# Kernel tuning notes

Measured on AMD Instinct MI355X. Metric: run time of the kernel, lower is better.

The kernel has to match this reference:

```python
import jax, jax.numpy as jnp
import numpy as np

B, S, E, H, FF = 4, 1024, 1024, 16, 4096
D = E // H
EPS = 1e-5


def layer_norm(x, g, b):
    m = jnp.mean(x, axis=-1, keepdims=True)
    v = jnp.var(x, axis=-1, keepdims=True)
    return (x - m) / jnp.sqrt(v + EPS) * g + b


def setup_inputs() -> dict:
    key = jax.random.key(0)
    ks = jax.random.split(key, 12)
    x = jax.random.normal(ks[0], (B, S, E), dtype=jnp.float32)
    # binary attention mask [B,S,S]; force diagonal=1 so no row is fully masked
    mask = jax.random.randint(ks[1], (B, S, S), 0, 2).astype(jnp.float32)
    idx = jnp.arange(S)
    mask = mask.at[:, idx, idx].set(1.0)
    gnn_adj = jax.random.normal(ks[2], (B, S, S), dtype=jnp.float32) * 0.02
    sc = 0.02
    params = dict(
        Wq=jax.random.normal(ks[3], (E, E), dtype=jnp.float32) * sc, bq=jnp.zeros((E,), jnp.float32),
        Wk=jax.random.normal(ks[4], (E, E), dtype=jnp.float32) * sc, bk=jnp.zeros((E,), jnp.float32),
        Wv=jax.random.normal(ks[5], (E, E), dtype=jnp.float32) * sc, bv=jnp.zeros((E,), jnp.float32),
        Wo=jax.random.normal(ks[6], (E, E), dtype=jnp.float32) * sc, bo=jnp.zeros((E,), jnp.float32),
        g1=jnp.ones((E,), jnp.float32), b1=jnp.zeros((E,), jnp.float32),
        g2=jnp.ones((E,), jnp.float32), b2=jnp.zeros((E,), jnp.float32),
        W1=jax.random.normal(ks[7], (E, FF), dtype=jnp.float32) * sc, bf1=jnp.zeros((FF,), jnp.float32),
        W2=jax.random.normal(ks[8], (FF, E), dtype=jnp.float32) * sc, bf2=jnp.zeros((E,), jnp.float32),
    )
    return dict(x=x, mask=mask, gnn_adj=gnn_adj, **params)


def reference(x, mask, gnn_adj, Wq, bq, Wk, bk, Wv, bv, Wo, bo, g1, b1, g2, b2, W1, bf1, W2, bf2):
    # pre-norm (norm_first=True), dropout = identity (eval)
    nx = layer_norm(x, g1, b1)
    # QKV projections -> [B,H,S,D]
    def split_heads(t):
        return t.reshape(B, S, H, D).transpose(0, 2, 1, 3)
    q = split_heads(nx @ Wq + bq)
    k = split_heads(nx @ Wk + bk)
    v = split_heads(nx @ Wv + bv)
    scores = jnp.einsum('bhqd,bhkd->bhqk', q, k) / jnp.sqrt(jnp.float32(D))
    m = mask[:, None]  # [B,1,S,S]
    scores = jnp.where(m == 0, -jnp.inf, scores * m)
    attn = jax.nn.softmax(scores, axis=-1)
    # non-standard: additive bias AFTER softmax
    attn = attn + gnn_adj[:, None]
    xv = jnp.einsum('bhqk,bhkd->bhqd', attn, v)
    xv = xv.transpose(0, 2, 1, 3).reshape(B, S, E)
    x = x + (xv @ Wo + bo)
    h = layer_norm(x, g2, b2)
    ff = jax.nn.gelu(h @ W1 + bf1, approximate=False) @ W2 + bf2
    return x + ff
```

## Files before the change

### kernel.cpp

```cpp
#include <hip/hip_runtime.h>
#include <hip/hip_bf16.h>

typedef unsigned short u16;
typedef short bf16x8 __attribute__((ext_vector_type(8)));
typedef float f32x4 __attribute__((ext_vector_type(4)));

#define B_ 4
#define S_ 1024
#define E_ 1024
#define H_ 16
#define FF_ 4096
#define D_ 64
#define M_ 4096

__device__ __forceinline__ u16 f2bf(float f) {
  unsigned int u = __builtin_bit_cast(unsigned int, f);
  u += 0x7fffu + ((u >> 16) & 1u);
  return (u16)(u >> 16);
}
__device__ __forceinline__ float bf2f(u16 v) {
  unsigned int u = ((unsigned int)v) << 16;
  return __builtin_bit_cast(float, u);
}

__device__ __forceinline__ void gld_lds16(const void* g, void* l) {
  __builtin_amdgcn_global_load_lds((__attribute__((address_space(1))) void*)g,
                                   (__attribute__((address_space(3))) void*)l,
                                   16, 0, 0);
}

__global__ void __launch_bounds__(256) pre_kernel(
    const float* __restrict__ wq, const float* __restrict__ wk,
    const float* __restrict__ wv, const float* __restrict__ wo,
    const float* __restrict__ w1, const float* __restrict__ w2,
    u16* __restrict__ wt,
    const float* __restrict__ x, const float* __restrict__ g1,
    const float* __restrict__ b1, u16* __restrict__ nx,
    const float* __restrict__ mask, const float* __restrict__ gnn,
    u16* __restrict__ biasI, u16* __restrict__ gnnbf) {
  __shared__ __attribute__((aligned(16))) float smem_f[1088];
  int bid = blockIdx.x;
  int t = threadIdx.x;
  if (bid < 12288) {
    const float* src; u16* dst; int K, N; int local;
    if (bid < 4096) {
      int wsel = bid >> 10; local = bid & 1023; K = 1024; N = 1024;
      src = wsel == 0 ? wq : wsel == 1 ? wk : wsel == 2 ? wv : wo;
      dst = wt + (size_t)wsel * 1024 * 1024;
    } else if (bid < 8192) {
      local = bid - 4096; K = 1024; N = 4096; src = w1;
      dst = wt + (size_t)4 * 1024 * 1024;
    } else {
      local = bid - 8192; K = 4096; N = 1024; src = w2;
      dst = wt + (size_t)8 * 1024 * 1024;
    }
    int tiles_n = N >> 5;
    int n0 = (local % tiles_n) << 5, k0 = (local / tiles_n) << 5;
    float (*tl)[33] = reinterpret_cast<float(*)[33]>(smem_f);
    int tx = t & 31, ty = t >> 5;
#pragma unroll
    for (int i = 0; i < 4; ++i)
      tl[ty + i * 8][tx] = src[(size_t)(k0 + ty + i * 8) * N + n0 + tx];
    __syncthreads();
#pragma unroll
    for (int i = 0; i < 4; ++i)
      dst[(size_t)(n0 + ty + i * 8) * K + k0 + tx] = f2bf(tl[tx][ty + i * 8]);
  } else if (bid < 16384) {
    int row = bid - 12288;
    const float* xr = x + (size_t)row * 1024;
    float4 v = *(const float4*)(xr + t * 4);
    float s = v.x + v.y + v.z + v.w;
    float q = v.x * v.x + v.y * v.y + v.z * v.z + v.w * v.w;
#pragma unroll
    for (int off = 1; off < 64; off <<= 1) {
      s += __shfl_xor(s, off);
      q += __shfl_xor(q, off);
    }
    float* sb = smem_f;
    float* qb = smem_f + 4;
    int w = t >> 6, l = t & 63;
    if (l == 0) { sb[w] = s; qb[w] = q; }
    __syncthreads();
    s = sb[0] + sb[1] + sb[2] + sb[3];
    q = qb[0] + qb[1] + qb[2] + qb[3];
    float mean = s * (1.f / 1024.f);
    float var = q * (1.f / 1024.f) - mean * mean;
    float rs = rsqrtf(var + 1e-5f);
    float4 gv = *(const float4*)(g1 + t * 4);
    float4 bv = *(const float4*)(b1 + t * 4);
    ushort4 o;
    o.x = f2bf((v.x - mean) * rs * gv.x + bv.x);
    o.y = f2bf((v.y - mean) * rs * gv.y + bv.y);
    o.z = f2bf((v.z - mean) * rs * gv.z + bv.z);
    o.w = f2bf((v.w - mean) * rs * gv.w + bv.w);
    *(ushort4*)(nx + (size_t)row * 1024 + t * 4) = o;
  } else {
    int row = bid - 16384;
    int b = row >> 10, q = row & 1023;
    float* mrow = smem_f;
    const float* mp = mask + ((size_t)row << 10);
    const float* gp = gnn + ((size_t)row << 10);
    float4 mv = *(const float4*)(mp + t * 4);
    *(float4*)(mrow + t * 4) = mv;
    float4 gv = *(const float4*)(gp + t * 4);
    ushort4 g4;
    g4.x = f2bf(gv.x); g4.y = f2bf(gv.y); g4.z = f2bf(gv.z); g4.w = f2bf(gv.w);
    *(ushort4*)(gnnbf + ((size_t)row << 10) + t * 4) = g4;
    __syncthreads();
    int kt = t >> 4, c = t & 15;
    const u16 NEG = f2bf(-30008.f);
    const u16 SHIFT = f2bf(-8.0f);
    ushort4 o;
    o.x = (mrow[kt * 64 + c] == 0.f) ? NEG : SHIFT;
    o.y = (mrow[kt * 64 + 16 + c] == 0.f) ? NEG : SHIFT;
    o.z = (mrow[kt * 64 + 32 + c] == 0.f) ? NEG : SHIFT;
    o.w = (mrow[kt * 64 + 48 + c] == 0.f) ? NEG : SHIFT;
    *(ushort4*)(biasI + (((size_t)(b * 16 + kt) << 10) + q) * 64 + c * 4) = o;
  }
}

__global__ void __launch_bounds__(256) vtrans_kernel(
    const u16* __restrict__ v, u16* __restrict__ vt) {
  int st = blockIdx.x, h = blockIdx.y, b = blockIdx.z;
  __shared__ u16 tl[64][72];
  const u16* src = v + ((((size_t)(b * 16 + h)) << 10) + (st << 6)) * 64;
  int r = threadIdx.x >> 2, g = (threadIdx.x & 3) << 4;
  *(uint4*)&tl[r][g] = *(const uint4*)(src + r * 64 + g);
  *(uint4*)&tl[r][g + 8] = *(const uint4*)(src + r * 64 + g + 8);
  __syncthreads();
  u16 tmp[16];
#pragma unroll
  for (int i = 0; i < 16; ++i) tmp[i] = tl[g + i][r];
  u16* dst = vt + ((size_t)b << 20) + (((size_t)(h * 64 + r)) << 10) + (st << 6) + g;
  *(uint4*)(dst) = *(uint4*)(tmp);
  *(uint4*)(dst + 8) = *(uint4*)(tmp + 8);
}

__global__ void __launch_bounds__(256) ln_kernel_b(
    const u16* __restrict__ x, const float* __restrict__ g,
    const float* __restrict__ bt, u16* __restrict__ out) {
  int row = blockIdx.x, t = threadIdx.x;
  const u16* xr = x + ((size_t)row << 10);
  ushort4 xv4 = *(const ushort4*)(xr + t * 4);
  float v0 = bf2f(xv4.x), v1 = bf2f(xv4.y), v2 = bf2f(xv4.z), v3 = bf2f(xv4.w);
  float s = v0 + v1 + v2 + v3;
  float q = v0 * v0 + v1 * v1 + v2 * v2 + v3 * v3;
#pragma unroll
  for (int off = 1; off < 64; off <<= 1) {
    s += __shfl_xor(s, off);
    q += __shfl_xor(q, off);
  }
  __shared__ float sb[4], qb[4];
  int w = t >> 6, l = t & 63;
  if (l == 0) { sb[w] = s; qb[w] = q; }
  __syncthreads();
  s = sb[0] + sb[1] + sb[2] + sb[3];
  q = qb[0] + qb[1] + qb[2] + qb[3];
  float mean = s * (1.f / 1024.f);
  float var = q * (1.f / 1024.f) - mean * mean;
  float rs = rsqrtf(var + 1e-5f);
  float4 gv = *(const float4*)(g + t * 4);
  float4 bv = *(const float4*)(bt + t * 4);
  ushort4 o;
  o.x = f2bf((v0 - mean) * rs * gv.x + bv.x);
  o.y = f2bf((v1 - mean) * rs * gv.y + bv.y);
  o.z = f2bf((v2 - mean) * rs * gv.z + bv.z);
  o.w = f2bf((v3 - mean) * rs * gv.w + bv.w);
  *(ushort4*)(out + ((size_t)row << 10) + t * 4) = o;
}

template <int LDA, int LDB, int NKT>
__device__ __forceinline__ void gemm_core_db64(
    const u16* __restrict__ A, const u16* __restrict__ Bt,
    int bm, int bn, u16* lds, f32x4 acc[4][2]) {
  const int tid = threadIdx.x;
  const int w = tid >> 6, l = tid & 63;
  const int wn = w << 5;
  const int lrow = l >> 3;
  const int cg = (l & 7) ^ lrow;
  const u16* Ab = A + (size_t)(bm << 6) * LDA + (cg << 3);
  const u16* Bb = Bt + (size_t)(bn << 7) * LDB + (cg << 3);
#define GSTAGE64(T, BUF)                                                     \
  {                                                                          \
    const int kk = (T) << 6;                                                 \
    u16* la = lds + (BUF) * 12288;                                           \
    u16* lb = la + 4096;                                                     \
    _Pragma("unroll") for (int i = 0; i < 2; ++i) {                          \
      int c = (w << 1) + i;                                                  \
      int row = (c << 3) + lrow;                                             \
      gld_lds16(Ab + (size_t)row * LDA + kk, la + (c << 9));                 \
    }                                                                        \
    _Pragma("unroll") for (int i = 0; i < 4; ++i) {                          \
      int c = (w << 2) + i;                                                  \
      int row = (c << 3) + lrow;                                             \
      gld_lds16(Bb + (size_t)row * LDB + kk, lb + (c << 9));                 \
    }                                                                        \
  }
  GSTAGE64(0, 0);
  __syncthreads();
  for (int t = 0; t < NKT; ++t) {
    if (t + 1 < NKT) GSTAGE64(t + 1, (t & 1) ^ 1);
    const u16* la = lds + (t & 1) * 12288;
    const u16* lb = la + 4096;
    bf16x8 af[2][4], bfr[2][2];
    const int rr = l & 15;
    const int kgb = l >> 4;
#pragma unroll
    for (int ks = 0; ks < 2; ++ks) {
      const int kg = kgb + (ks << 2);
#pragma unroll
      for (int f = 0; f < 4; ++f) {
        int ra = (f << 4) + rr;
        af[ks][f] = *(const bf16x8*)(la + (ra << 6) + ((kg ^ (ra & 7)) << 3));
      }
#pragma unroll
      for (int f = 0; f < 2; ++f) {
        int rb = wn + (f << 4) + rr;
        bfr[ks][f] = *(const bf16x8*)(lb + (rb << 6) + ((kg ^ (rb & 7)) << 3));
      }
    }
#pragma unroll
    for (int fm = 0; fm < 4; ++fm)
#pragma unroll
      for (int fn = 0; fn < 2; ++fn)
#pragma unroll
        for (int ks = 0; ks < 2; ++ks)
          acc[fm][fn] = __builtin_amdgcn_mfma_f32_16x16x32_bf16(
              af[ks][fm], bfr[ks][fn], acc[fm][fn], 0, 0, 0);
    __syncthreads();
  }
#undef GSTAGE64
}

template <int LDA, int LDB, int NKT>
__device__ __forceinline__ void gemm_core_p3(
    const u16* __restrict__ A, const u16* __restrict__ Bt,
    int bm, int bn, u16* lds, f32x4 acc[4][2]) {
  const int tid = threadIdx.x;
  const int w = tid >> 6, l = tid & 63;
  const int wn = w << 5;
  const int lrow = l >> 3;
  const int cg = (l & 7) ^ lrow;
  const u16* Ab = A + (size_t)(bm << 6) * LDA + (cg << 3);
  const u16* Bb = Bt + (size_t)(bn << 7) * LDB + (cg << 3);
#define PSTAGE(T, BUF)                                                       \
  {                                                                          \
    const int kk = (T) << 6;                                                 \
    u16* la = lds + (BUF) * 12288;                                           \
    u16* lb = la + 4096;                                                     \
    _Pragma("unroll") for (int i = 0; i < 2; ++i) {                          \
      int c = (w << 1) + i;                                                  \
      int row = (c << 3) + lrow;                                             \
      gld_lds16(Ab + (size_t)row * LDA + kk, la + (c << 9));                 \
    }                                                                        \
    _Pragma("unroll") for (int i = 0; i < 4; ++i) {                          \
      int c = (w << 2) + i;                                                  \
      int row = (c << 3) + lrow;                                             \
      gld_lds16(Bb + (size_t)row * LDB + kk, lb + (c << 9));                 \
    }                                                                        \
  }
  PSTAGE(0, 0);
  PSTAGE(1, 1);
  int cur = 0;
  for (int t = 0; t < NKT; ++t) {
    if (t + 2 < NKT) {
      int nb = cur + 2; if (nb >= 3) nb -= 3;
      PSTAGE(t + 2, nb);
      asm volatile("s_waitcnt vmcnt(12)" ::: "memory");
    } else if (t + 1 < NKT) {
      asm volatile("s_waitcnt vmcnt(6)" ::: "memory");
    } else {
      asm volatile("s_waitcnt vmcnt(0)" ::: "memory");
    }
    __builtin_amdgcn_sched_barrier(0);
    __builtin_amdgcn_s_barrier();
    const u16* la = lds + cur * 12288;
    const u16* lb = la + 4096;
    bf16x8 af[2][4], bfr[2][2];
    const int rr = l & 15;
    const int kgb = l >> 4;
#pragma unroll
    for (int ks = 0; ks < 2; ++ks) {
      const int kg = kgb + (ks << 2);
#pragma unroll
      for (int f = 0; f < 4; ++f) {
        int ra = (f << 4) + rr;
        af[ks][f] = *(const bf16x8*)(la + (ra << 6) + ((kg ^ (ra & 7)) << 3));
      }
#pragma unroll
      for (int f = 0; f < 2; ++f) {
        int rb = wn + (f << 4) + rr;
        bfr[ks][f] = *(const bf16x8*)(lb + (rb << 6) + ((kg ^ (rb & 7)) << 3));
      }
    }
    __builtin_amdgcn_s_setprio(1);
#pragma unroll
    for (int fm = 0; fm < 4; ++fm)
#pragma unroll
      for (int fn = 0; fn < 2; ++fn)
#pragma unroll
        for (int ks = 0; ks < 2; ++ks)
          acc[fm][fn] = __builtin_amdgcn_mfma_f32_16x16x32_bf16(
              af[ks][fm], bfr[ks][fn], acc[fm][fn], 0, 0, 0);
    __builtin_amdgcn_s_setprio(0);
    asm volatile("s_waitcnt lgkmcnt(0)" ::: "memory");
    __builtin_amdgcn_sched_barrier(0);
    __builtin_amdgcn_s_barrier();
    cur = (cur == 2) ? 0 : cur + 1;
  }
#undef PSTAGE
}

#define ACC_INIT64()                      \
  f32x4 acc[4][2];                        \
  { f32x4 zf = {0.f, 0.f, 0.f, 0.f};      \
_Pragma("unroll")                         \
    for (int a = 0; a < 4; ++a)           \
_Pragma("unroll")                         \
      for (int bb = 0; bb < 2; ++bb) acc[a][bb] = zf; }

#define EPI_SETUP64()                                   \
  const int w = threadIdx.x >> 6, l = threadIdx.x & 63; \
  const int wn = w << 5;

#define GEMM_LDS64()  __shared__ __attribute__((aligned(16))) u16 lds[2 * 12288]

__global__ void __launch_bounds__(256, 2) gemm_qkv(
    const u16* __restrict__ nx, const u16* __restrict__ wt,
    const float* __restrict__ bq, const float* __restrict__ bk,
    const float* __restrict__ bv, u16* __restrict__ qk, u16* __restrict__ vtmp) {
  GEMM_LDS64();
  ACC_INIT64();
  int z = blockIdx.z;
  const u16* Bt = wt + (size_t)z * 1024 * 1024;
  const float* bias = z == 0 ? bq : z == 1 ? bk : bv;
  u16* out = z == 2 ? vtmp : qk + (size_t)z * M_ * 1024;
  const float scl = (z == 0) ? 0.18033688f : 1.0f;
  gemm_core_db64<1024, 1024, 16>(nx, Bt, blockIdx.x, blockIdx.y, lds, acc);
  EPI_SETUP64();
#pragma unroll
  for (int fm = 0; fm < 4; ++fm)
#pragma unroll
    for (int fn = 0; fn < 2; ++fn)
#pragma unroll
      for (int j = 0; j < 4; ++j) {
        int row = (blockIdx.x << 6) + (fm << 4) + ((l >> 4) << 2) + j;
        int col = (blockIdx.y << 7) + wn + (fn << 4) + (l & 15);
        float v = (acc[fm][fn][j] + bias[col]) * scl;
        int b = row >> 10, s = row & 1023;
        int h = col >> 6, d = col & 63;
        out[(((size_t)(b * 16 + h) << 10) + s) * 64 + d] = f2bf(v);
      }
}

__global__ void __launch_bounds__(256, 2) gemm_gnnv(
    const u16* __restrict__ gnnbf, const u16* __restrict__ vt,
    u16* __restrict__ xvg) {
  GEMM_LDS64();
  ACC_INIT64();
  int b = blockIdx.z;
  const u16* A = gnnbf + ((size_t)b << 20);
  const u16* Bt = vt + ((size_t)b << 20);
  u16* out = xvg + ((size_t)b << 20);
  gemm_core_db64<1024, 1024, 16>(A, Bt, blockIdx.x, blockIdx.y, lds, acc);
  EPI_SETUP64();
#pragma unroll
  for (int fm = 0; fm < 4; ++fm)
#pragma unroll
    for (int fn = 0; fn < 2; ++fn)
#pragma unroll
      for (int j = 0; j < 4; ++j) {
        int row = (blockIdx.x << 6) + (fm << 4) + ((l >> 4) << 2) + j;
        int col = (blockIdx.y << 7) + wn + (fn << 4) + (l & 15);
        out[((size_t)row << 10) + col] = f2bf(acc[fm][fn][j]);
      }
}

__global__ void __launch_bounds__(256, 2) gemm_wo(
    const u16* __restrict__ xv, const u16* __restrict__ wt,
    const float* __restrict__ bo, const float* __restrict__ xres,
    u16* __restrict__ x1b) {
  GEMM_LDS64();
  ACC_INIT64();
  gemm_core_db64<1024, 1024, 16>(xv, wt, blockIdx.x, blockIdx.y, lds, acc);
  EPI_SETUP64();
#pragma unroll
  for (int fm = 0; fm < 4; ++fm)
#pragma unroll
    for (int fn = 0; fn < 2; ++fn)
#pragma unroll
      for (int j = 0; j < 4; ++j) {
        int row = (blockIdx.x << 6) + (fm << 4) + ((l >> 4) << 2) + j;
        int col = (blockIdx.y << 7) + wn + (fn << 4) + (l & 15);
        size_t idx = ((size_t)row << 10) + col;
        x1b[idx] = f2bf(acc[fm][fn][j] + bo[col] + xres[idx]);
      }
}

__global__ void __launch_bounds__(512, 1) gemm_w1_256p(
    const u16* __restrict__ hb, const u16* __restrict__ wt,
    const float* __restrict__ bf1, u16* __restrict__ ff1) {
  extern __shared__ __attribute__((aligned(16))) u16 lds[];
  const int bid = blockIdx.x;
  const int lin = ((bid & 7) << 5) + (bid >> 3);
  const int bm = lin & 15, bn = lin >> 4;
  const int tid = threadIdx.x;
  const int w = tid >> 6, l = tid & 63;
  const int wm = (w >> 2) << 7;
  const int wn = (w & 3) << 6;
  const int lrow3 = l >> 3;
  const int vsw = (l & 7) ^ lrow3;
  const int rpar = vsw >> 2, k8s = vsw & 3;
  const u16* Ab = hb + (size_t)(bm << 8) * 1024 + k8s * 8;
  const u16* Bb = wt + (size_t)(bn << 8) * 1024 + k8s * 8;

  f32x4 acc[8][4];
  {
    f32x4 zf = {0.f, 0.f, 0.f, 0.f};
#pragma unroll
    for (int a = 0; a < 8; ++a)
#pragma unroll
      for (int bb2 = 0; bb2 < 4; ++bb2) acc[a][bb2] = zf;
  }

#define WSTAGE(T, BUF)                                                       \
  {                                                                          \
    const int kk = (T) << 5;                                                 \
    u16* la = lds + (BUF) * 16384;                                           \
    u16* lb = la + 8192;                                                     \
    _Pragma("unroll") for (int i = 0; i < 2; ++i) {                          \
      int c = (w << 1) + i;                                                  \
      int row = ((c << 3) + lrow3) * 2 + rpar;                               \
      gld_lds16(Ab + (size_t)row * 1024 + kk, la + (c << 9) + (l << 3));     \
      gld_lds16(Bb + (size_t)row * 1024 + kk, lb + (c << 9) + (l << 3));     \
    }                                                                        \
  }

  WSTAGE(0, 0);
  WSTAGE(1, 1);
  int cur = 0;
  const int rr = l & 15;
  const int kg = l >> 4;
  for (int t = 0; t < 32; ++t) {
    if (t + 2 < 32) {
      int nb = cur + 2; if (nb >= 3) nb -= 3;
      WSTAGE(t + 2, nb);
      asm volatile("s_waitcnt vmcnt(8)" ::: "memory");
    } else if (t + 1 < 32) {
      asm volatile("s_waitcnt vmcnt(4)" ::: "memory");
    } else {
      asm volatile("s_waitcnt vmcnt(0)" ::: "memory");
    }
    __builtin_amdgcn_sched_barrier(0);
    __builtin_amdgcn_s_barrier();
    const u16* la = lds + cur * 16384;
    const u16* lb = la + 8192;
    bf16x8 bfr[4];
#pragma unroll
    for (int fn = 0; fn < 4; ++fn) {
      int rb = wn + (fn << 4) + rr;
      int slot = (((rb & 1) << 2) | kg) ^ ((rb >> 1) & 7);
      bfr[fn] = *(const bf16x8*)(lb + ((rb >> 1) << 6) + (slot << 3));
    }
    __builtin_amdgcn_s_setprio(1);
#pragma unroll
    for (int fm = 0; fm < 8; ++fm) {
      int ra = wm + (fm << 4) + rr;
      int slot = (((ra & 1) << 2) | kg) ^ ((ra >> 1) & 7);
      bf16x8 afr = *(const bf16x8*)(la + ((ra >> 1) << 6) + (slot << 3));
#pragma unroll
      for (int fn = 0; fn < 4; ++fn)
        acc[fm][fn] = __builtin_amdgcn_mfma_f32_16x16x32_bf16(
            afr, bfr[fn], acc[fm][fn], 0, 0, 0);
    }
    __builtin_amdgcn_s_setprio(0);
    asm volatile("s_waitcnt lgkmcnt(0)" ::: "memory");
    __builtin_amdgcn_sched_barrier(0);
    __builtin_amdgcn_s_barrier();
    cur = (cur == 2) ? 0 : cur + 1;
  }
#undef WSTAGE
#pragma unroll
  for (int fm = 0; fm < 8; ++fm)
#pragma unroll
    for (int fn = 0; fn < 4; ++fn)
#pragma unroll
      for (int j = 0; j < 4; ++j) {
        int row = (bm << 8) + wm + (fm << 4) + ((l >> 4) << 2) + j;
        int col = (bn << 8) + wn + (fn << 4) + (l & 15);
        float v = acc[fm][fn][j] + bf1[col];
        float ge = 0.5f * v * (1.f + erff(v * 0.70710678118654752f));
        ff1[((size_t)row << 12) + col] = f2bf(ge);
      }
}

__global__ void __launch_bounds__(256, 2) gemm_w2(
    const u16* __restrict__ ff1, const u16* __restrict__ wt,
    const float* __restrict__ bf2, const u16* __restrict__ x1b,
    float* __restrict__ out) {
  extern __shared__ __attribute__((aligned(16))) u16 lds[];
  ACC_INIT64();
  gemm_core_p3<4096, 4096, 64>(ff1, wt, blockIdx.x, blockIdx.y, lds, acc);
  EPI_SETUP64();
#pragma unroll
  for (int fm = 0; fm < 4; ++fm)
#pragma unroll
    for (int fn = 0; fn < 2; ++fn)
#pragma unroll
      for (int j = 0; j < 4; ++j) {
        int row = (blockIdx.x << 6) + (fm << 4) + ((l >> 4) << 2) + j;
        int col = (blockIdx.y << 7) + wn + (fn << 4) + (l & 15);
        size_t idx = ((size_t)row << 10) + col;
        out[idx] = acc[fm][fn][j] + bf2[col] + bf2f(x1b[idx]);
      }
}

__global__ void __launch_bounds__(256, 2) attn_kernel(
    const u16* __restrict__ Q, const u16* __restrict__ K,
    const u16* __restrict__ Vt, const u16* __restrict__ biasI,
    const u16* __restrict__ xvg, u16* __restrict__ xv) {
  const int lin = ((blockIdx.x & 7) << 6) + (blockIdx.x >> 3);
  const int qt = lin & 7, h = (lin >> 3) & 15, b = lin >> 7;
  const int tid = threadIdx.x, w = tid >> 6, l = tid & 63;
  __shared__ __attribute__((aligned(16))) u16 kbuf[2][64 * 64];
  __shared__ __attribute__((aligned(16))) u16 vbuf[2][64 * 64];
  __shared__ __attribute__((aligned(16))) u16 pbuf[4][32 * 64];
  const size_t bh = ((size_t)(b * 16 + h)) << 16;
  const u16* Qb = Q + bh;
  const u16* Kb = K + bh;
  const u16* Vtb = Vt + ((size_t)b << 20) + ((size_t)(h * 64) << 10);
  const u16* biasb = biasI + ((size_t)b << 20);
  const int q0 = (qt << 7) + (w << 5);
  const int lrow = l >> 3, cg = (l & 7) ^ lrow;
  const int l4 = l >> 4, lo = l & 15;
  u16* p_w = pbuf[w];

  bf16x8 qf[2][2];
#pragma unroll
  for (int m = 0; m < 2; ++m)
#pragma unroll
    for (int ks = 0; ks < 2; ++ks)
      qf[m][ks] = *(const bf16x8*)(Qb + ((size_t)(q0 + m * 16 + lo) << 6) +
                                   l4 * 8 + ks * 32);
  bf16x8 onesf;
#pragma unroll
  for (int j = 0; j < 8; ++j) onesf[j] = (short)0x3F80;

  f32x4 osoft[2][4], osum[2];
  f32x4 zf = {0.f, 0.f, 0.f, 0.f};
#pragma unroll
  for (int m = 0; m < 2; ++m) {
    osum[m] = zf;
#pragma unroll
    for (int fd = 0; fd < 4; ++fd) osoft[m][fd] = zf;
  }

#define STAGE(T, BUF)                                                          \
  {                                                                            \
    int kv0s = (T) << 6;                                                       \
    u16* kd = &kbuf[BUF][0];                                                   \
    u16* vd = &vbuf[BUF][0];                                                   \
    _Pragma("unroll") for (int i = 0; i < 2; ++i) {                            \
      int c = (w << 1) + i;                                                    \
      gld_lds16(Kb + ((size_t)(kv0s + (c << 3) + lrow) << 6) + (cg << 3),      \
                kd + (c << 9));                                                \
      gld_lds16(Vtb + ((size_t)((c << 3) + lrow) << 10) + kv0s + (cg << 3),    \
                vd + (c << 9));                                                \
    }                                                                          \
  }

  STAGE(0, 0);
  __syncthreads();

  for (int t = 0; t < 16; ++t) {
    const int cur = t & 1;
    if (t < 15) STAGE(t + 1, cur ^ 1);
    const u16* kb_ = &kbuf[cur][0];
    const u16* vb_ = &vbuf[cur][0];
    f32x4 sacc[2][4];
#pragma unroll
    for (int m = 0; m < 2; ++m)
#pragma unroll
      for (int j = 0; j < 4; ++j) {
        ushort4 bb = *(const ushort4*)(
            biasb + (((size_t)(t * 1024 + q0 + m * 16 + l4 * 4 + j)) << 6) +
            lo * 4);
        sacc[m][0][j] = bf2f(bb.x);
        sacc[m][1][j] = bf2f(bb.y);
        sacc[m][2][j] = bf2f(bb.z);
        sacc[m][3][j] = bf2f(bb.w);
      }
    __builtin_amdgcn_s_setprio(1);
#pragma unroll
    for (int ks = 0; ks < 2; ++ks) {
      const int kg = l4 + (ks << 2);
      bf16x8 kf[4];
#pragma unroll
      for (int fn = 0; fn < 4; ++fn) {
        int rk = (fn << 4) + lo;
        kf[fn] = *(const bf16x8*)(kb_ + (rk << 6) + ((kg ^ (rk & 7)) << 3));
      }
#pragma unroll
      for (int m = 0; m < 2; ++m)
#pragma unroll
        for (int fn = 0; fn < 4; ++fn)
          sacc[m][fn] = __builtin_amdgcn_mfma_f32_16x16x32_bf16(
              qf[m][ks], kf[fn], sacc[m][fn], 0, 0, 0);
    }
    __builtin_amdgcn_s_setprio(0);
#pragma unroll
    for (int m = 0; m < 2; ++m)
#pragma unroll
      for (int fn = 0; fn < 4; ++fn)
#pragma unroll
        for (int j = 0; j < 4; ++j) {
          float p = exp2f(sacc[m][fn][j]);
          unsigned int u = __builtin_bit_cast(unsigned int, p);
          int prow = (m << 4) + (l4 << 2) + j;
          int pcol = (fn << 4) + lo;
          p_w[(prow << 6) + (pcol ^ ((prow & 7) << 3))] =
              (u16)((u + 0x8000u) >> 16);
        }
    __builtin_amdgcn_s_setprio(1);
#pragma unroll
    for (int ks = 0; ks < 2; ++ks) {
      const int kg = l4 + (ks << 2);
      bf16x8 pf[2], vf[4];
#pragma unroll
      for (int m = 0; m < 2; ++m) {
        int pr = (m << 4) + lo;
        pf[m] = *(const bf16x8*)(p_w + (pr << 6) + ((kg ^ (pr & 7)) << 3));
      }
#pragma unroll
      for (int fd = 0; fd < 4; ++fd) {
        int rd = (fd << 4) + lo;
        vf[fd] = *(const bf16x8*)(vb_ + (rd << 6) + ((kg ^ (rd & 7)) << 3));
      }
#pragma unroll
      for (int m = 0; m < 2; ++m) {
        osum[m] = __builtin_amdgcn_mfma_f32_16x16x32_bf16(
            pf[m], onesf, osum[m], 0, 0, 0);
#pragma unroll
        for (int fd = 0; fd < 4; ++fd)
          osoft[m][fd] = __builtin_amdgcn_mfma_f32_16x16x32_bf16(
              pf[m], vf[fd], osoft[m][fd], 0, 0, 0);
      }
    }
    __builtin_amdgcn_s_setprio(0);
    __syncthreads();
  }
#pragma unroll
  for (int m = 0; m < 2; ++m) {
    f32x4 rl;
#pragma unroll
    for (int j = 0; j < 4; ++j) rl[j] = 1.0f / osum[m][j];
#pragma unroll
    for (int fd = 0; fd < 4; ++fd)
#pragma unroll
      for (int j = 0; j < 4; ++j) {
        int qrow = q0 + (m << 4) + (l4 << 2) + j;
        int e = (h << 6) + (fd << 4) + lo;
        size_t idx = (((size_t)(b * 1024 + qrow)) << 10) + e;
        float o = osoft[m][fd][j] * rl[j] + bf2f(xvg[idx]);
        xv[idx] = f2bf(o);
      }
  }
#undef STAGE
}

extern "C" void kernel_launch(void* const* d_in, const int* in_sizes, int n_in,
                              void* d_out, int out_size, void* d_ws, size_t ws_size,
                              hipStream_t stream) {
  (void)in_sizes; (void)n_in; (void)out_size; (void)ws_size;
  const float* x   = (const float*)d_in[0];
  const float* mask= (const float*)d_in[1];
  const float* gnn = (const float*)d_in[2];
  const float* Wq  = (const float*)d_in[3];
  const float* bq  = (const float*)d_in[4];
  const float* Wk  = (const float*)d_in[5];
  const float* bk  = (const float*)d_in[6];
  const float* Wv  = (const float*)d_in[7];
  const float* bv  = (const float*)d_in[8];
  const float* Wo  = (const float*)d_in[9];
  const float* bo  = (const float*)d_in[10];
  const float* g1  = (const float*)d_in[11];
  const float* b1  = (const float*)d_in[12];
  const float* g2  = (const float*)d_in[13];
  const float* b2  = (const float*)d_in[14];
  const float* W1  = (const float*)d_in[15];
  const float* bf1 = (const float*)d_in[16];
  const float* W2  = (const float*)d_in[17];
  const float* bf2 = (const float*)d_in[18];
  float* out = (float*)d_out;

  char* ws = (char*)d_ws;
  const size_t MB = 1024 * 1024;
  u16*  wt    = (u16*)(ws);
  u16*  nx    = (u16*)(ws + 24 * MB);
  u16*  xvbuf = (u16*)(ws + 24 * MB);
  u16*  hbuf  = (u16*)(ws + 24 * MB);
  u16*  qk    = (u16*)(ws + 32 * MB);
  u16*  vt    = (u16*)(ws + 48 * MB);
  u16*  biasI = (u16*)(ws + 56 * MB);
  u16*  gnnbf = (u16*)(ws + 64 * MB);
  u16*  x1b   = (u16*)(ws + 64 * MB);
  u16*  vtmp  = (u16*)(ws + 72 * MB);
  u16*  xvg   = (u16*)(ws + 72 * MB);
  u16*  ff1   = (u16*)(ws + 32 * MB);

  pre_kernel<<<20480, 256, 0, stream>>>(Wq, Wk, Wv, Wo, W1, W2, wt,
                                        x, g1, b1, nx, mask, gnn, biasI, gnnbf);
  gemm_qkv<<<dim3(64, 8, 3), 256, 0, stream>>>(nx, wt, bq, bk, bv, qk, vtmp);
  vtrans_kernel<<<dim3(16, 16, 4), 256, 0, stream>>>(vtmp, vt);
  gemm_gnnv<<<dim3(16, 8, 4), 256, 0, stream>>>(gnnbf, vt, xvg);
  attn_kernel<<<512, 256, 0, stream>>>(
      qk, qk + (size_t)4 * MB, vt, biasI, xvg, xvbuf);
  gemm_wo<<<dim3(64, 8), 256, 0, stream>>>(xvbuf, wt + (size_t)3 * MB, bo, x, x1b);
  ln_kernel_b<<<4096, 256, 0, stream>>>(x1b, g2, b2, hbuf);
  gemm_w1_256p<<<256, 512, 3 * 32768, stream>>>(hbuf, wt + (size_t)4 * MB, bf1, ff1);
  gemm_w2<<<dim3(64, 8), 256, 3 * 24576, stream>>>(ff1, wt + (size_t)8 * MB, bf2, x1b, out);
}
```

Before: 229.9 us.

## Bit-pack attention mask, fuse V transpose into QKV GEMM, simplify W1 GEMM

```diff
diff --git a/kernel.cpp b/kernel.cpp
--- a/kernel.cpp
+++ b/kernel.cpp
@@ -4,6 +4,7 @@
 typedef unsigned short u16;
 typedef short bf16x8 __attribute__((ext_vector_type(8)));
 typedef float f32x4 __attribute__((ext_vector_type(4)));
+typedef unsigned long long u64;
 
 #define B_ 4
 #define S_ 1024
@@ -37,7 +38,7 @@
     const float* __restrict__ x, const float* __restrict__ g1,
     const float* __restrict__ b1, u16* __restrict__ nx,
     const float* __restrict__ mask, const float* __restrict__ gnn,
-    u16* __restrict__ biasI, u16* __restrict__ gnnbf) {
+    u64* __restrict__ mb, u16* __restrict__ gnnbf) {
   __shared__ __attribute__((aligned(16))) float smem_f[1088];
   int bid = blockIdx.x;
   int t = threadIdx.x;
@@ -97,43 +98,29 @@
   } else {
     int row = bid - 16384;
     int b = row >> 10, q = row & 1023;
-    float* mrow = smem_f;
     const float* mp = mask + ((size_t)row << 10);
     const float* gp = gnn + ((size_t)row << 10);
     float4 mv = *(const float4*)(mp + t * 4);
-    *(float4*)(mrow + t * 4) = mv;
     float4 gv = *(const float4*)(gp + t * 4);
     ushort4 g4;
     g4.x = f2bf(gv.x); g4.y = f2bf(gv.y); g4.z = f2bf(gv.z); g4.w = f2bf(gv.w);
     *(ushort4*)(gnnbf + ((size_t)row << 10) + t * 4) = g4;
-    __syncthreads();
-    int kt = t >> 4, c = t & 15;
-    const u16 NEG = f2bf(-30008.f);
-    const u16 SHIFT = f2bf(-8.0f);
-    ushort4 o;
-    o.x = (mrow[kt * 64 + c] == 0.f) ? NEG : SHIFT;
-    o.y = (mrow[kt * 64 + 16 + c] == 0.f) ? NEG : SHIFT;
-    o.z = (mrow[kt * 64 + 32 + c] == 0.f) ? NEG : SHIFT;
-    o.w = (mrow[kt * 64 + 48 + c] == 0.f) ? NEG : SHIFT;
-    *(ushort4*)(biasI + (((size_t)(b * 16 + kt) << 10) + q) * 64 + c * 4) = o;
-  }
-}
-
-__global__ void __launch_bounds__(256) vtrans_kernel(
-    const u16* __restrict__ v, u16* __restrict__ vt) {
-  int st = blockIdx.x, h = blockIdx.y, b = blockIdx.z;
-  __shared__ u16 tl[64][72];
-  const u16* src = v + ((((size_t)(b * 16 + h)) << 10) + (st << 6)) * 64;
-  int r = threadIdx.x >> 2, g = (threadIdx.x & 3) << 4;
-  *(uint4*)&tl[r][g] = *(const uint4*)(src + r * 64 + g);
-  *(uint4*)&tl[r][g + 8] = *(const uint4*)(src + r * 64 + g + 8);
-  __syncthreads();
-  u16 tmp[16];
-#pragma unroll
-  for (int i = 0; i < 16; ++i) tmp[i] = tl[g + i][r];
-  u16* dst = vt + ((size_t)b << 20) + (((size_t)(h * 64 + r)) << 10) + (st << 6) + g;
-  *(uint4*)(dst) = *(uint4*)(tmp);
-  *(uint4*)(dst + 8) = *(uint4*)(tmp + 8);
+    u64 b0 = __ballot(mv.x != 0.f);
+    u64 b1v = __ballot(mv.y != 0.f);
+    u64 b2 = __ballot(mv.z != 0.f);
+    u64 b3 = __ballot(mv.w != 0.f);
+    int L = t & 63;
+    if ((L & 15) == 0) {
+      int m = L >> 4;
+      int sh = m << 4;
+      u64 W = ((b0 >> sh) & 0xFFFFull)
+            | (((b1v >> sh) & 0xFFFFull) << 16)
+            | (((b2 >> sh) & 0xFFFFull) << 32)
+            | (((b3 >> sh) & 0xFFFFull) << 48);
+      int kt = ((t >> 6) << 2) + m;
+      mb[(((size_t)(b * 16 + kt)) << 10) + q] = W;
+    }
+  }
 }
 
 __global__ void __launch_bounds__(256) ln_kernel_b(
@@ -328,29 +315,55 @@
 __global__ void __launch_bounds__(256, 2) gemm_qkv(
     const u16* __restrict__ nx, const u16* __restrict__ wt,
     const float* __restrict__ bq, const float* __restrict__ bk,
-    const float* __restrict__ bv, u16* __restrict__ qk, u16* __restrict__ vtmp) {
+    const float* __restrict__ bv, u16* __restrict__ qk, u16* __restrict__ vt) {
   GEMM_LDS64();
   ACC_INIT64();
   int z = blockIdx.z;
   const u16* Bt = wt + (size_t)z * 1024 * 1024;
   const float* bias = z == 0 ? bq : z == 1 ? bk : bv;
-  u16* out = z == 2 ? vtmp : qk + (size_t)z * M_ * 1024;
   const float scl = (z == 0) ? 0.18033688f : 1.0f;
   gemm_core_db64<1024, 1024, 16>(nx, Bt, blockIdx.x, blockIdx.y, lds, acc);
   EPI_SETUP64();
-#pragma unroll
-  for (int fm = 0; fm < 4; ++fm)
-#pragma unroll
-    for (int fn = 0; fn < 2; ++fn)
-#pragma unroll
-      for (int j = 0; j < 4; ++j) {
-        int row = (blockIdx.x << 6) + (fm << 4) + ((l >> 4) << 2) + j;
-        int col = (blockIdx.y << 7) + wn + (fn << 4) + (l & 15);
-        float v = (acc[fm][fn][j] + bias[col]) * scl;
-        int b = row >> 10, s = row & 1023;
-        int h = col >> 6, d = col & 63;
-        out[(((size_t)(b * 16 + h) << 10) + s) * 64 + d] = f2bf(v);
-      }
+  if (z == 2) {
+    u16 (*tl)[72] = (u16(*)[72])lds;
+#pragma unroll
+    for (int fm = 0; fm < 4; ++fm)
+#pragma unroll
+      for (int fn = 0; fn < 2; ++fn)
+#pragma unroll
+        for (int j = 0; j < 4; ++j) {
+          int rloc = (fm << 4) + ((l >> 4) << 2) + j;
+          int cloc = wn + (fn << 4) + (l & 15);
+          int col = (blockIdx.y << 7) + cloc;
+          tl[cloc][rloc] = f2bf(acc[fm][fn][j] + bias[col]);
+        }
+    __syncthreads();
+    int col = threadIdx.x >> 1, half = threadIdx.x & 1;
+    int e = (blockIdx.y << 7) + col;
+    int rowg = (blockIdx.x << 6) + (half << 5);
+    int b = rowg >> 10, s0 = rowg & 1023;
+    u16* dst = vt + ((size_t)b << 20) + ((size_t)e << 10) + s0;
+    const u16* srcl = &tl[col][half << 5];
+    *(uint4*)(dst)      = *(const uint4*)(srcl);
+    *(uint4*)(dst + 8)  = *(const uint4*)(srcl + 8);
+    *(uint4*)(dst + 16) = *(const uint4*)(srcl + 16);
+    *(uint4*)(dst + 24) = *(const uint4*)(srcl + 24);
+  } else {
+    u16* out = qk + (size_t)z * M_ * 1024;
+#pragma unroll
+    for (int fm = 0; fm < 4; ++fm)
+#pragma unroll
+      for (int fn = 0; fn < 2; ++fn)
+#pragma unroll
+        for (int j = 0; j < 4; ++j) {
+          int row = (blockIdx.x << 6) + (fm << 4) + ((l >> 4) << 2) + j;
+          int col = (blockIdx.y << 7) + wn + (fn << 4) + (l & 15);
+          float v = (acc[fm][fn][j] + bias[col]) * scl;
+          int b = row >> 10, s = row & 1023;
+          int h = col >> 6, d = col & 63;
+          out[(((size_t)(b * 16 + h) << 10) + s) * 64 + d] = f2bf(v);
+        }
+  }
 }
 
 __global__ void __launch_bounds__(256, 2) gemm_gnnv(
@@ -397,97 +410,21 @@
       }
 }
 
-__global__ void __launch_bounds__(512, 1) gemm_w1_256p(
+__global__ void __launch_bounds__(256, 2) gemm_w1(
     const u16* __restrict__ hb, const u16* __restrict__ wt,
     const float* __restrict__ bf1, u16* __restrict__ ff1) {
-  extern __shared__ __attribute__((aligned(16))) u16 lds[];
-  const int bid = blockIdx.x;
-  const int lin = ((bid & 7) << 5) + (bid >> 3);
-  const int bm = lin & 15, bn = lin >> 4;
-  const int tid = threadIdx.x;
-  const int w = tid >> 6, l = tid & 63;
-  const int wm = (w >> 2) << 7;
-  const int wn = (w & 3) << 6;
-  const int lrow3 = l >> 3;
-  const int vsw = (l & 7) ^ lrow3;
-  const int rpar = vsw >> 2, k8s = vsw & 3;
-  const u16* Ab = hb + (size_t)(bm << 8) * 1024 + k8s * 8;
-  const u16* Bb = wt + (size_t)(bn << 8) * 1024 + k8s * 8;
-
-  f32x4 acc[8][4];
-  {
-    f32x4 zf = {0.f, 0.f, 0.f, 0.f};
-#pragma unroll
-    for (int a = 0; a < 8; ++a)
-#pragma unroll
-      for (int bb2 = 0; bb2 < 4; ++bb2) acc[a][bb2] = zf;
-  }
-
-#define WSTAGE(T, BUF)                                                       \
-  {                                                                          \
-    const int kk = (T) << 5;                                                 \
-    u16* la = lds + (BUF) * 16384;                                           \
-    u16* lb = la + 8192;                                                     \
-    _Pragma("unroll") for (int i = 0; i < 2; ++i) {                          \
-      int c = (w << 1) + i;                                                  \
-      int row = ((c << 3) + lrow3) * 2 + rpar;                               \
-      gld_lds16(Ab + (size_t)row * 1024 + kk, la + (c << 9) + (l << 3));     \
-      gld_lds16(Bb + (size_t)row * 1024 + kk, lb + (c << 9) + (l << 3));     \
-    }                                                                        \
-  }
-
-  WSTAGE(0, 0);
-  WSTAGE(1, 1);
-  int cur = 0;
-  const int rr = l & 15;
-  const int kg = l >> 4;
-  for (int t = 0; t < 32; ++t) {
-    if (t + 2 < 32) {
-      int nb = cur + 2; if (nb >= 3) nb -= 3;
-      WSTAGE(t + 2, nb);
-      asm volatile("s_waitcnt vmcnt(8)" ::: "memory");
-    } else if (t + 1 < 32) {
-      asm volatile("s_waitcnt vmcnt(4)" ::: "memory");
-    } else {
-      asm volatile("s_waitcnt vmcnt(0)" ::: "memory");
-    }
-    __builtin_amdgcn_sched_barrier(0);
-    __builtin_amdgcn_s_barrier();
-    const u16* la = lds + cur * 16384;
-    const u16* lb = la + 8192;
-    bf16x8 bfr[4];
-#pragma unroll
-    for (int fn = 0; fn < 4; ++fn) {
-      int rb = wn + (fn << 4) + rr;
-      int slot = (((rb & 1) << 2) | kg) ^ ((rb >> 1) & 7);
-      bfr[fn] = *(const bf16x8*)(lb + ((rb >> 1) << 6) + (slot << 3));
-    }
-    __builtin_amdgcn_s_setprio(1);
-#pragma unroll
-    for (int fm = 0; fm < 8; ++fm) {
-      int ra = wm + (fm << 4) + rr;
-      int slot = (((ra & 1) << 2) | kg) ^ ((ra >> 1) & 7);
-      bf16x8 afr = *(const bf16x8*)(la + ((ra >> 1) << 6) + (slot << 3));
-#pragma unroll
-      for (int fn = 0; fn < 4; ++fn)
-        acc[fm][fn] = __builtin_amdgcn_mfma_f32_16x16x32_bf16(
-            afr, bfr[fn], acc[fm][fn], 0, 0, 0);
-    }
-    __builtin_amdgcn_s_setprio(0);
-    asm volatile("s_waitcnt lgkmcnt(0)" ::: "memory");
-    __builtin_amdgcn_sched_barrier(0);
-    __builtin_amdgcn_s_barrier();
-    cur = (cur == 2) ? 0 : cur + 1;
-  }
-#undef WSTAGE
-#pragma unroll
-  for (int fm = 0; fm < 8; ++fm)
-#pragma unroll
-    for (int fn = 0; fn < 4; ++fn)
+  GEMM_LDS64();
+  ACC_INIT64();
+  gemm_core_db64<1024, 1024, 16>(hb, wt, blockIdx.x, blockIdx.y, lds, acc);
+  EPI_SETUP64();
+#pragma unroll
+  for (int fm = 0; fm < 4; ++fm)
+#pragma unroll
+    for (int fn = 0; fn < 2; ++fn)
 #pragma unroll
       for (int j = 0; j < 4; ++j) {
-        int row = (bm << 8) + wm + (fm << 4) + ((l >> 4) << 2) + j;
-        int col = (bn << 8) + wn + (fn << 4) + (l & 15);
+        int row = (blockIdx.x << 6) + (fm << 4) + ((l >> 4) << 2) + j;
+        int col = (blockIdx.y << 7) + wn + (fn << 4) + (l & 15);
         float v = acc[fm][fn][j] + bf1[col];
         float ge = 0.5f * v * (1.f + erff(v * 0.70710678118654752f));
         ff1[((size_t)row << 12) + col] = f2bf(ge);
@@ -517,7 +454,7 @@
 
 __global__ void __launch_bounds__(256, 2) attn_kernel(
     const u16* __restrict__ Q, const u16* __restrict__ K,
-    const u16* __restrict__ Vt, const u16* __restrict__ biasI,
+    const u16* __restrict__ Vt, const u64* __restrict__ mb,
     const u16* __restrict__ xvg, u16* __restrict__ xv) {
   const int lin = ((blockIdx.x & 7) << 6) + (blockIdx.x >> 3);
   const int qt = lin & 7, h = (lin >> 3) & 15, b = lin >> 7;
@@ -529,11 +466,13 @@
   const u16* Qb = Q + bh;
   const u16* Kb = K + bh;
   const u16* Vtb = Vt + ((size_t)b << 20) + ((size_t)(h * 64) << 10);
-  const u16* biasb = biasI + ((size_t)b << 20);
+  const u64* mbb = mb + (((size_t)(b * 16)) << 10);
   const int q0 = (qt << 7) + (w << 5);
   const int lrow = l >> 3, cg = (l & 7) ^ lrow;
   const int l4 = l >> 4, lo = l & 15;
+  const int p0 = ((lo & 3) << 4) + (lo >> 2);
   u16* p_w = pbuf[w];
+  const float FU = -8.0f, FM = -30008.0f;
 
   bf16x8 qf[2][2];
 #pragma unroll
@@ -577,18 +516,18 @@
     if (t < 15) STAGE(t + 1, cur ^ 1);
     const u16* kb_ = &kbuf[cur][0];
     const u16* vb_ = &vbuf[cur][0];
+    const u64* mbt = mbb + (((size_t)t) << 10);
     f32x4 sacc[2][4];
 #pragma unroll
     for (int m = 0; m < 2; ++m)
 #pragma unroll
       for (int j = 0; j < 4; ++j) {
-        ushort4 bb = *(const ushort4*)(
-            biasb + (((size_t)(t * 1024 + q0 + m * 16 + l4 * 4 + j)) << 6) +
-            lo * 4);
-        sacc[m][0][j] = bf2f(bb.x);
-        sacc[m][1][j] = bf2f(bb.y);
-        sacc[m][2][j] = bf2f(bb.z);
-        sacc[m][3][j] = bf2f(bb.w);
+        u64 wb = mbt[q0 + (m << 4) + (l4 << 2) + j];
+        unsigned int bits = (unsigned int)(wb >> p0);
+        sacc[m][0][j] = (bits & 1u) ? FU : FM;
+        sacc[m][1][j] = (bits & 16u) ? FU : FM;
+        sacc[m][2][j] = (bits & 256u) ? FU : FM;
+        sacc[m][3][j] = (bits & 4096u) ? FU : FM;
       }
     __builtin_amdgcn_s_setprio(1);
 #pragma unroll
@@ -701,22 +640,20 @@
   u16*  hbuf  = (u16*)(ws + 24 * MB);
   u16*  qk    = (u16*)(ws + 32 * MB);
   u16*  vt    = (u16*)(ws + 48 * MB);
-  u16*  biasI = (u16*)(ws + 56 * MB);
+  u64*  mb    = (u64*)(ws + 56 * MB);
   u16*  gnnbf = (u16*)(ws + 64 * MB);
   u16*  x1b   = (u16*)(ws + 64 * MB);
-  u16*  vtmp  = (u16*)(ws + 72 * MB);
   u16*  xvg   = (u16*)(ws + 72 * MB);
   u16*  ff1   = (u16*)(ws + 32 * MB);
 
   pre_kernel<<<20480, 256, 0, stream>>>(Wq, Wk, Wv, Wo, W1, W2, wt,
-                                        x, g1, b1, nx, mask, gnn, biasI, gnnbf);
-  gemm_qkv<<<dim3(64, 8, 3), 256, 0, stream>>>(nx, wt, bq, bk, bv, qk, vtmp);
-  vtrans_kernel<<<dim3(16, 16, 4), 256, 0, stream>>>(vtmp, vt);
+                                        x, g1, b1, nx, mask, gnn, mb, gnnbf);
+  gemm_qkv<<<dim3(64, 8, 3), 256, 0, stream>>>(nx, wt, bq, bk, bv, qk, vt);
   gemm_gnnv<<<dim3(16, 8, 4), 256, 0, stream>>>(gnnbf, vt, xvg);
   attn_kernel<<<512, 256, 0, stream>>>(
-      qk, qk + (size_t)4 * MB, vt, biasI, xvg, xvbuf);
+      qk, qk + (size_t)4 * MB, vt, mb, xvg, xvbuf);
   gemm_wo<<<dim3(64, 8), 256, 0, stream>>>(xvbuf, wt + (size_t)3 * MB, bo, x, x1b);
   ln_kernel_b<<<4096, 256, 0, stream>>>(x1b, g2, b2, hbuf);
-  gemm_w1_256p<<<256, 512, 3 * 32768, stream>>>(hbuf, wt + (size_t)4 * MB, bf1, ff1);
+  gemm_w1<<<dim3(64, 32), 256, 0, stream>>>(hbuf, wt + (size_t)4 * MB, bf1, ff1);
   gemm_w2<<<dim3(64, 8), 256, 3 * 24576, stream>>>(ff1, wt + (size_t)8 * MB, bf2, x1b, out);
 }
```

Result: no change. 226.4 us, median of 2 (-1.5%).
